# Kernel optimization log

Hardware: AMD Instinct MI355X
Metric: run time of the kernel (lower is better)

## Reference

```python
import jax, jax.numpy as jnp
import numpy as np

B, N, D = 64, 577, 768
H = 12
HD = D // H
TOP_K_RATIO = 0.1


def setup_inputs() -> dict:
    key = jax.random.key(0)
    ks = jax.random.split(key, 8)
    s = 1.0 / np.sqrt(D)
    return {
        "x": jax.random.normal(ks[0], (B, N, D), jnp.float32),
        "accumulated_attention": jax.random.uniform(ks[1], (B, N, N), jnp.float32),
        "q_w": jax.random.normal(ks[2], (D, D), jnp.float32) * s,
        "k_w": jax.random.normal(ks[3], (D, D), jnp.float32) * s,
        "v_w": jax.random.normal(ks[4], (D, D), jnp.float32) * s,
        "proj_w": jax.random.normal(ks[5], (D, D), jnp.float32) * s,
        "proj_b": jnp.zeros((D,), jnp.float32),
    }


def reference(x, accumulated_attention, q_w, k_w, v_w, proj_w, proj_b):
    b, n, d = x.shape
    scale = HD ** -0.5
    # CLS-to-patch attention rollout row: (B, N-1)
    cls_attn = accumulated_attention[:, 0, 1:]
    # projections -> (B, H, N, HD)
    q = (x @ q_w.T).reshape(b, n, H, HD).transpose(0, 2, 1, 3)
    k = (x @ k_w.T).reshape(b, n, H, HD).transpose(0, 2, 1, 3)
    v = (x @ v_w.T).reshape(b, n, H, HD).transpose(0, 2, 1, 3)
    # top-k patch selection (+1 for CLS offset), prepend CLS index 0
    kk = max(1, int((n - 1) * TOP_K_RATIO))
    _, top_idx = jax.lax.top_k(cls_attn, kk)
    sel = jnp.concatenate([jnp.zeros((b, 1), top_idx.dtype), top_idx + 1], axis=1)  # (B, K+1)
    # gather selected queries: (B, H, K+1, HD)
    local_q = jnp.take_along_axis(q, sel[:, None, :, None], axis=2)
    # cross-attention of local queries against full K/V
    attn = jax.nn.softmax(jnp.einsum("bhkd,bhnd->bhkn", local_q, k) * scale, axis=-1)
    local_out = jnp.einsum("bhkn,bhnd->bhkd", attn, v)
    local_out = local_out.transpose(0, 2, 1, 3).reshape(b, -1, d)  # (B, K+1, D)
    # scatter back into a copy of x (indices are unique per batch)
    out = x.at[jnp.arange(b)[:, None], sel].set(local_out)
    return out @ proj_w.T + proj_b
```

## Files before the change

kernel.cpp:

```cpp
#include <hip/hip_runtime.h>
#include <stdint.h>

typedef unsigned short u16;
typedef short bf16x8 __attribute__((ext_vector_type(8)));
typedef float f32x4 __attribute__((ext_vector_type(4)));

__device__ __forceinline__ float b2f(u16 u){
  unsigned int i = ((unsigned int)u) << 16;
  return __builtin_bit_cast(float, i);
}
__device__ __forceinline__ u16 f2b(float f){
  unsigned int i = __builtin_bit_cast(unsigned int, f);
  i += 0x7FFFu + ((i >> 16) & 1u);
  return (u16)(i >> 16);
}

__device__ __forceinline__ void async16(const void* g, void* l){
  __builtin_amdgcn_global_load_lds((__attribute__((address_space(1))) void*)(void*)g,
                                   (__attribute__((address_space(3))) void*)l, 16, 0, 0);
}

__global__ void probe_kernel(const u16* __restrict__ qw, int* __restrict__ flag){
  int cnt = 0;
  for (int i = threadIdx.x; i < 4096; i += 64){
    int e = (qw[i] >> 7) & 0xFF;
    cnt += (e >= 140);
  }
#pragma unroll
  for (int off = 32; off; off >>= 1) cnt += __shfl_down(cnt, off);
  if (threadIdx.x == 0) *flag = (cnt > 64) ? 1 : 0;
}

__global__ __launch_bounds__(256) void cvt_kernel(const void* __restrict__ src,
                                                  u16* __restrict__ dst, int n,
                                                  const int* __restrict__ flagp){
  const int i = (blockIdx.x * 256 + threadIdx.x) * 8;
  if (i >= n) return;
  if (*flagp){
    f32x4 a = *(const f32x4*)((const float*)src + i);
    f32x4 b = *(const f32x4*)((const float*)src + i + 4);
    bf16x8 v;
#pragma unroll
    for (int j = 0; j < 4; ++j){ v[j] = (short)f2b(a[j]); v[4+j] = (short)f2b(b[j]); }
    *(bf16x8*)(dst + i) = v;
  } else {
    *(bf16x8*)(dst + i) = *(const bf16x8*)((const u16*)src + i);
  }
}

__global__ __launch_bounds__(256) void cvtw4_kernel(const void* __restrict__ s0,
                                                    const void* __restrict__ s1,
                                                    const void* __restrict__ s2,
                                                    const void* __restrict__ s3,
                                                    u16* __restrict__ dst,
                                                    const int* __restrict__ flagp){
  const int b = blockIdx.x;
  const int wsel = b / 288;
  const int i = (b - wsel*288) * 2048 + threadIdx.x * 8;
  const void* src = (wsel == 0) ? s0 : (wsel == 1) ? s1 : (wsel == 2) ? s2 : s3;
  u16* d = dst + (size_t)wsel * 589824 + i;
  if (*flagp){
    f32x4 a = *(const f32x4*)((const float*)src + i);
    f32x4 c = *(const f32x4*)((const float*)src + i + 4);
    bf16x8 v;
#pragma unroll
    for (int j = 0; j < 4; ++j){ v[j] = (short)f2b(a[j]); v[4+j] = (short)f2b(c[j]); }
    *(bf16x8*)d = v;
  } else {
    *(bf16x8*)d = *(const bf16x8*)((const u16*)src + i);
  }
}

__global__ void cvtb_kernel(const void* __restrict__ src, float* __restrict__ dst,
                            int n, const int* __restrict__ flagp){
  int i = blockIdx.x * 256 + threadIdx.x;
  if (i < n) dst[i] = *flagp ? ((const float*)src)[i] : b2f(((const u16*)src)[i]);
}

__global__ __launch_bounds__(576) void topk_kernel(const void* __restrict__ aa,
                                                   int* __restrict__ qrows,
                                                   const int* __restrict__ flagp){
  const int b = blockIdx.x;
  const int isf32 = *flagp;
  __shared__ float vals[576];
  const int i = threadIdx.x;
  const size_t off = (size_t)b*332929 + 1 + i;
  vals[i] = isf32 ? ((const float*)aa)[off] : b2f(((const u16*)aa)[off]);
  __syncthreads();
  const float vi = vals[i];
  int rank = 0;
  for (int j = 0; j < 576; ++j){
    float vj = vals[j];
    rank += (int)((vj > vi) || (vj == vi && j < i));
  }
  if (rank < 57) qrows[b*58 + 1 + rank] = b*577 + i + 1;
  if (i == 0)    qrows[b*58] = b*577;
}

__global__ __launch_bounds__(256) void gemm_bt(
    const u16* __restrict__ A, const u16* __restrict__ W,
    u16* __restrict__ Ck, u16* __restrict__ Cvt, float* __restrict__ Cout,
    u16* __restrict__ Clq,
    const int* __restrict__ qrows, const float* __restrict__ bias, int mode)
{
  __shared__ __align__(16) u16 As0[4096], As1[4096], As2[4096];
  __shared__ __align__(16) u16 Bs0[4096], Bs1[4096], Bs2[4096];
  const int tid = threadIdx.x;
  const int w = tid >> 6, l = tid & 63;

  int bx, by; bool lqp = false;
  if (mode == 0){
    const int bid = blockIdx.x;
    const int wg = (bid & 7) * 672 + (bid >> 3);
    if (wg < 5202){ bx = wg % 18; by = wg / 18; }
    else { const int t = wg - 5202; bx = t % 6; by = t / 6; lqp = true; }
  } else { bx = blockIdx.x; by = blockIdx.y; }

  const int mBase = by * 128;
  const int nBase = bx * 128;
  const int Meff  = (mode == 0 && !lqp) ? 36928 : 3712;

  const int r0 = tid >> 2;
  const int kc = (((tid & 3) ^ ((r0 >> 1) & 3)) * 8);
  int arow0 = mBase + r0;       if (arow0 > Meff-1) arow0 = Meff-1;
  int arow1 = mBase + 64 + r0;  if (arow1 > Meff-1) arow1 = Meff-1;
  if (mode == 0 && lqp){ arow0 = qrows[arow0]; arow1 = qrows[arow1]; }
  const int wrowBase = (mode == 0 && !lqp) ? (768 + nBase) : nBase;
  const u16* ag0 = A + (size_t)arow0 * 768 + kc;
  const u16* ag1 = A + (size_t)arow1 * 768 + kc;
  const u16* bg0 = W + (size_t)(wrowBase + r0) * 768 + kc;
  const u16* bg1 = W + (size_t)(wrowBase + 64 + r0) * 768 + kc;
  const int toff0 = tid * 8, toff1 = (256 + tid) * 8;

  f32x4 acc[4][4] = {};
  const int wm = (w >> 1) * 64, wn = (w & 1) * 64;
  const int lm = l & 15;
  const int lkx = (((l >> 4) ^ ((l >> 1) & 3)) * 8);

#define STAGE(Ab, Bb, koff) do { \
    async16(ag0 + (koff), &Ab[toff0]); \
    async16(ag1 + (koff), &Ab[toff1]); \
    async16(bg0 + (koff), &Bb[toff0]); \
    async16(bg1 + (koff), &Bb[toff1]); } while(0)

#define COMPUTE(Ab, Bb) { \
    bf16x8 af[4], bfr[4]; \
    _Pragma("unroll") \
    for (int i = 0; i < 4; ++i) af[i]  = *(const bf16x8*)&Ab[(wm + i*16 + lm)*32 + lkx]; \
    _Pragma("unroll") \
    for (int j = 0; j < 4; ++j) bfr[j] = *(const bf16x8*)&Bb[(wn + j*16 + lm)*32 + lkx]; \
    __builtin_amdgcn_s_setprio(1); \
    _Pragma("unroll") \
    for (int i = 0; i < 4; ++i) \
      _Pragma("unroll") \
      for (int j = 0; j < 4; ++j) \
        acc[i][j] = __builtin_amdgcn_mfma_f32_16x16x32_bf16(af[i], bfr[j], acc[i][j], 0, 0, 0); \
    __builtin_amdgcn_s_setprio(0); }

#define VMW4 asm volatile("s_waitcnt vmcnt(4)" ::: "memory")
#define VMW0 asm volatile("s_waitcnt vmcnt(0)" ::: "memory")
#define BAR  __builtin_amdgcn_s_barrier()

  STAGE(As0, Bs0, 0);
  STAGE(As1, Bs1, 32);
#pragma unroll
  for (int u = 0; u < 7; ++u){
    const int kb = u * 96;
    VMW4; BAR; STAGE(As2, Bs2, kb + 64);  COMPUTE(As0, Bs0);
    VMW4; BAR; STAGE(As0, Bs0, kb + 96);  COMPUTE(As1, Bs1);
    VMW4; BAR; STAGE(As1, Bs1, kb + 128); COMPUTE(As2, Bs2);
  }
  VMW4; BAR; STAGE(As2, Bs2, 736); COMPUTE(As0, Bs0);
  VMW4; BAR;                       COMPUTE(As1, Bs1);
  VMW0; BAR;                       COMPUTE(As2, Bs2);

#undef STAGE
#undef COMPUTE
#undef VMW4
#undef VMW0
#undef BAR

  if (mode == 1){
#pragma unroll
    for (int i = 0; i < 4; ++i){
#pragma unroll
      for (int r = 0; r < 4; ++r){
        int m = mBase + wm + i*16 + ((l >> 4) << 2) + r;
        if (m < 3712){
          size_t base = (size_t)qrows[m] * 768;
#pragma unroll
          for (int j = 0; j < 4; ++j){
            int n = nBase + wn + j*16 + lm;
            Cout[base + n] = acc[i][j][r] + bias[n];
          }
        }
      }
    }
    return;
  }
  if (lqp){
#pragma unroll
    for (int i = 0; i < 4; ++i){
#pragma unroll
      for (int r = 0; r < 4; ++r){
        int m = mBase + wm + i*16 + ((l >> 4) << 2) + r;
#pragma unroll
        for (int j = 0; j < 4; ++j){
          int n = nBase + wn + j*16 + lm;
          Clq[(size_t)m*768 + n] = f2b(acc[i][j][r]);
        }
      }
    }
  } else if (nBase < 768){
#pragma unroll
    for (int i = 0; i < 4; ++i){
#pragma unroll
      for (int r = 0; r < 4; ++r){
        int m = mBase + wm + i*16 + ((l >> 4) << 2) + r;
        if (m < 36928){
#pragma unroll
          for (int j = 0; j < 4; ++j){
            int n = nBase + wn + j*16 + lm;
            Ck[(size_t)m*768 + n] = f2b(acc[i][j][r]);
          }
        }
      }
    }
  } else if (nBase < 1536){
#pragma unroll
    for (int i = 0; i < 4; ++i){
#pragma unroll
      for (int r = 0; r < 4; ++r){
        int m = mBase + wm + i*16 + ((l >> 4) << 2) + r;
        if (m < 36928){
          int bb = m / 577;
          int nn = m - bb*577;
#pragma unroll
          for (int j = 0; j < 4; ++j){
            int nf = nBase - 768 + wn + j*16 + lm;
            Cvt[((size_t)(bb*12 + (nf >> 6))*64 + (nf & 63))*608 + nn] = f2b(acc[i][j][r]);
          }
        }
      }
    }
  } else {
#pragma unroll
    for (int i = 0; i < 4; ++i){
#pragma unroll
      for (int r = 0; r < 4; ++r){
        int m = mBase + wm + i*16 + ((l >> 4) << 2) + r;
        if (m < 36928){
          size_t base = (size_t)m * 768;
#pragma unroll
          for (int j = 0; j < 4; ++j){
            int nf = nBase - 1536 + wn + j*16 + lm;
            Cout[base + nf] = acc[i][j][r] + bias[nf];
          }
        }
      }
    }
  }
}

#define SLD 580
__global__ __launch_bounds__(256) void attn_kernel(
    const u16* __restrict__ lq, const u16* __restrict__ K,
    const u16* __restrict__ Vt, u16* __restrict__ lout)
{
  const int bid = blockIdx.x;
  const int wg = (bid & 7) * 384 + (bid >> 3);
  const int mt = wg & 3;
  const int hb = wg >> 2;
  const int h = hb % 12, b = hb / 12;

  __shared__ __align__(16) u16 qs[16*64];
  __shared__ __align__(16) float S[16*SLD];
  float* red = (float*)qs;
  const int tid = threadIdx.x, w = tid >> 6, l = tid & 63;
  const int lm = l & 15, lk = (l >> 4) * 8;

  for (int idx = tid; idx < 1024; idx += 256){
    int r = idx >> 6, c = idx & 63;
    int gm = mt*16 + r;
    qs[idx] = (gm < 58) ? lq[((size_t)b*58 + gm)*768 + h*64 + c] : (u16)0;
  }
  __syncthreads();
  bf16x8 aq0 = *(const bf16x8*)&qs[lm*64 + lk];
  bf16x8 aq1 = *(const bf16x8*)&qs[lm*64 + 32 + lk];

  const u16* Kb = K + (size_t)b*577*768 + h*64;
  for (int t = w; t < 37; t += 4){
    int n0 = t*16;
    int n = n0 + lm; if (n > 576) n = 576;
    const u16* kp = Kb + (size_t)n*768;
    bf16x8 b0 = *(const bf16x8*)&kp[lk];
    bf16x8 b1 = *(const bf16x8*)&kp[32 + lk];
    f32x4 c = {};
    c = __builtin_amdgcn_mfma_f32_16x16x32_bf16(aq0, b0, c, 0, 0, 0);
    c = __builtin_amdgcn_mfma_f32_16x16x32_bf16(aq1, b1, c, 0, 0, 0);
    if (n0 + lm < 577){
#pragma unroll
      for (int r = 0; r < 4; ++r)
        S[(((l >> 4) << 2) + r)*SLD + n0 + lm] = c[r] * 0.125f;
    }
  }
  __syncthreads();

  const int row = tid >> 4, g = tid & 15;
  float mx = -1e30f;
  for (int n = g; n < 577; n += 16) mx = fmaxf(mx, S[row*SLD + n]);
  red[row*17 + g] = mx;
  __syncthreads();
  float m2 = red[row*17];
#pragma unroll
  for (int i = 1; i < 16; ++i) m2 = fmaxf(m2, red[row*17 + i]);
  float sum = 0.f;
  for (int n = g; n < 577; n += 16){
    float e = __expf(S[row*SLD + n] - m2);
    S[row*SLD + n] = e;
    sum += e;
  }
  __syncthreads();
  red[row*17 + g] = sum;
  __syncthreads();
  float s2 = 0.f;
#pragma unroll
  for (int i = 0; i < 16; ++i) s2 += red[row*17 + i];
  float inv = 1.f / s2;
  for (int n = g; n < 577; n += 16) S[row*SLD + n] *= inv;
  __syncthreads();

  const u16* Vb = Vt + ((size_t)(b*12 + h) * 64) * 608;
  f32x4 oc = {};
  for (int ks = 0; ks < 18; ++ks){
    int kb = ks*32 + lk;
    f32x4 p0 = *(const f32x4*)&S[lm*SLD + kb];
    f32x4 p1 = *(const f32x4*)&S[lm*SLD + kb + 4];
    bf16x8 af;
#pragma unroll
    for (int j = 0; j < 4; ++j){ af[j] = (short)f2b(p0[j]); af[4+j] = (short)f2b(p1[j]); }
    bf16x8 bv = *(const bf16x8*)&Vb[(size_t)(w*16 + lm)*608 + kb];
    oc = __builtin_amdgcn_mfma_f32_16x16x32_bf16(af, bv, oc, 0, 0, 0);
  }
  {
    float vt576 = b2f(Vb[(size_t)(w*16 + lm)*608 + 576]);
#pragma unroll
    for (int r = 0; r < 4; ++r)
      oc[r] += S[(((l >> 4) << 2) + r)*SLD + 576] * vt576;
  }
#pragma unroll
  for (int r = 0; r < 4; ++r){
    int ml = mt*16 + ((l >> 4) << 2) + r;
    if (ml < 58)
      lout[((size_t)b*58 + ml)*768 + h*64 + w*16 + lm] = f2b(oc[r]);
  }
}

extern "C" void kernel_launch(void* const* d_in, const int* in_sizes, int n_in,
                              void* d_out, int out_size, void* d_ws, size_t ws_size,
                              hipStream_t stream)
{
  const void* x    = d_in[0];
  const void* aacc = d_in[1];
  const void* q_w  = d_in[2];
  const void* k_w  = d_in[3];
  const void* v_w  = d_in[4];
  const void* p_w  = d_in[5];
  const void* p_b  = d_in[6];

  const int M  = 36928;
  const int Ms = 3712;
  const int XE = M * 768;
  const int WE = 768 * 768;

  u16* Kbuf = (u16*)d_ws;
  u16* Vt   = Kbuf + (size_t)M * 768;
  u16* lq   = Vt + (size_t)768 * 64 * 608;
  u16* lout = lq + (size_t)Ms * 768;
  u16* xb   = lout + (size_t)Ms * 768;
  u16* qwb  = xb + (size_t)XE;
  u16* pwb  = qwb + (size_t)3 * WE;
  float* biasf = (float*)(qwb + (size_t)4 * WE);
  int* qrows = (int*)(biasf + 768);
  int* flagp = qrows + 3712;

  probe_kernel<<<1, 64, 0, stream>>>((const u16*)q_w, flagp);
  cvt_kernel<<<XE/8/256, 256, 0, stream>>>(x, xb, XE, flagp);
  cvtw4_kernel<<<1152, 256, 0, stream>>>(q_w, k_w, v_w, p_w, qwb, flagp);
  cvtb_kernel<<<3, 256, 0, stream>>>(p_b, biasf, 768, flagp);
  topk_kernel<<<64, 576, 0, stream>>>(aacc, qrows, flagp);

  gemm_bt<<<5376, 256, 0, stream>>>(xb, qwb, Kbuf, Vt, (float*)d_out, lq,
                                    qrows, biasf, 0);
  attn_kernel<<<3072, 256, 0, stream>>>(lq, Kbuf, Vt, lout);
  gemm_bt<<<dim3(6, 29), 256, 0, stream>>>(lout, pwb, nullptr, nullptr,
                                           (float*)d_out, nullptr, qrows, biasf, 1);
}
```

Before: 578.2 us.

## Double-buffer GEMM for occupancy, prefetch K/V in attention, defer softmax normalization

The GEMM drops from triple- to double-buffered LDS staging, with an extra barrier between compute and restage, and adds a launch-bounds occupancy hint of 4 blocks. The aim is more resident workgroups per CU in exchange for a shallower prefetch pipeline. The attention kernel software-prefetches the next K tile and the next V fragment into registers. It also skips the pass that normalizes the softmax row and instead multiplies the output by the reciprocal row sum at the end. Unnormalized probabilities are then rounded to bf16 before the PV MFMA, which slightly changes precision.

Result: no change. 576.0 us (-0.4%).

```diff
diff --git a/kernel.cpp b/kernel.cpp
--- a/kernel.cpp
+++ b/kernel.cpp
@@ -97,14 +97,14 @@
   if (i == 0)    qrows[b*58] = b*577;
 }
 
-__global__ __launch_bounds__(256) void gemm_bt(
+__global__ __launch_bounds__(256, 4) void gemm_bt(
     const u16* __restrict__ A, const u16* __restrict__ W,
     u16* __restrict__ Ck, u16* __restrict__ Cvt, float* __restrict__ Cout,
     u16* __restrict__ Clq,
     const int* __restrict__ qrows, const float* __restrict__ bias, int mode)
 {
-  __shared__ __align__(16) u16 As0[4096], As1[4096], As2[4096];
-  __shared__ __align__(16) u16 Bs0[4096], Bs1[4096], Bs2[4096];
+  __shared__ __align__(16) u16 As0[4096], As1[4096];
+  __shared__ __align__(16) u16 Bs0[4096], Bs1[4096];
   const int tid = threadIdx.x;
   const int w = tid >> 6, l = tid & 63;
 
@@ -164,15 +164,12 @@
   STAGE(As0, Bs0, 0);
   STAGE(As1, Bs1, 32);
 #pragma unroll
-  for (int u = 0; u < 7; ++u){
-    const int kb = u * 96;
-    VMW4; BAR; STAGE(As2, Bs2, kb + 64);  COMPUTE(As0, Bs0);
-    VMW4; BAR; STAGE(As0, Bs0, kb + 96);  COMPUTE(As1, Bs1);
-    VMW4; BAR; STAGE(As1, Bs1, kb + 128); COMPUTE(As2, Bs2);
-  }
-  VMW4; BAR; STAGE(As2, Bs2, 736); COMPUTE(As0, Bs0);
-  VMW4; BAR;                       COMPUTE(As1, Bs1);
-  VMW0; BAR;                       COMPUTE(As2, Bs2);
+  for (int u = 0; u < 11; ++u){
+    VMW4; BAR; COMPUTE(As0, Bs0); BAR; STAGE(As0, Bs0, u*64 + 64);
+    VMW4; BAR; COMPUTE(As1, Bs1); BAR; STAGE(As1, Bs1, u*64 + 96);
+  }
+  VMW4; BAR; COMPUTE(As0, Bs0);
+  VMW0; BAR; COMPUTE(As1, Bs1);
 
 #undef STAGE
 #undef COMPUTE
@@ -275,7 +272,8 @@
 
   __shared__ __align__(16) u16 qs[16*64];
   __shared__ __align__(16) float S[16*SLD];
-  float* red = (float*)qs;
+  float* red  = (float*)qs;
+  float* invp = red + 16*17;
   const int tid = threadIdx.x, w = tid >> 6, l = tid & 63;
   const int lm = l & 15, lk = (l >> 4) * 8;
 
@@ -289,19 +287,31 @@
   bf16x8 aq1 = *(const bf16x8*)&qs[lm*64 + 32 + lk];
 
   const u16* Kb = K + (size_t)b*577*768 + h*64;
-  for (int t = w; t < 37; t += 4){
-    int n0 = t*16;
-    int n = n0 + lm; if (n > 576) n = 576;
+  {
+    int t = w;
+    int n = t*16 + lm; if (n > 576) n = 576;
     const u16* kp = Kb + (size_t)n*768;
-    bf16x8 b0 = *(const bf16x8*)&kp[lk];
-    bf16x8 b1 = *(const bf16x8*)&kp[32 + lk];
-    f32x4 c = {};
-    c = __builtin_amdgcn_mfma_f32_16x16x32_bf16(aq0, b0, c, 0, 0, 0);
-    c = __builtin_amdgcn_mfma_f32_16x16x32_bf16(aq1, b1, c, 0, 0, 0);
-    if (n0 + lm < 577){
-#pragma unroll
-      for (int r = 0; r < 4; ++r)
-        S[(((l >> 4) << 2) + r)*SLD + n0 + lm] = c[r] * 0.125f;
+    bf16x8 kb0 = *(const bf16x8*)&kp[lk];
+    bf16x8 kb1 = *(const bf16x8*)&kp[32 + lk];
+    while (t < 37){
+      const int tn = t + 4;
+      bf16x8 nb0 = kb0, nb1 = kb1;
+      if (tn < 37){
+        int n2 = tn*16 + lm; if (n2 > 576) n2 = 576;
+        const u16* kp2 = Kb + (size_t)n2*768;
+        nb0 = *(const bf16x8*)&kp2[lk];
+        nb1 = *(const bf16x8*)&kp2[32 + lk];
+      }
+      f32x4 c = {};
+      c = __builtin_amdgcn_mfma_f32_16x16x32_bf16(aq0, kb0, c, 0, 0, 0);
+      c = __builtin_amdgcn_mfma_f32_16x16x32_bf16(aq1, kb1, c, 0, 0, 0);
+      const int n0 = t*16;
+      if (n0 + lm < 577){
+#pragma unroll
+        for (int r = 0; r < 4; ++r)
+          S[(((l >> 4) << 2) + r)*SLD + n0 + lm] = c[r] * 0.125f;
+      }
+      kb0 = nb0; kb1 = nb1; t = tn;
     }
   }
   __syncthreads();
@@ -323,30 +333,37 @@
   __syncthreads();
   red[row*17 + g] = sum;
   __syncthreads();
-  float s2 = 0.f;
-#pragma unroll
-  for (int i = 0; i < 16; ++i) s2 += red[row*17 + i];
-  float inv = 1.f / s2;
-  for (int n = g; n < 577; n += 16) S[row*SLD + n] *= inv;
+  if (g == 0){
+    float s2 = 0.f;
+#pragma unroll
+    for (int i = 0; i < 16; ++i) s2 += red[row*17 + i];
+    invp[row] = 1.f / s2;
+  }
   __syncthreads();
 
   const u16* Vb = Vt + ((size_t)(b*12 + h) * 64) * 608;
+  const u16* Vrow = Vb + (size_t)(w*16 + lm)*608;
   f32x4 oc = {};
+  bf16x8 bv = *(const bf16x8*)&Vrow[lk];
   for (int ks = 0; ks < 18; ++ks){
-    int kb = ks*32 + lk;
+    const int kb = ks*32 + lk;
+    bf16x8 bvn = bv;
+    if (ks < 17) bvn = *(const bf16x8*)&Vrow[kb + 32];
     f32x4 p0 = *(const f32x4*)&S[lm*SLD + kb];
     f32x4 p1 = *(const f32x4*)&S[lm*SLD + kb + 4];
     bf16x8 af;
 #pragma unroll
     for (int j = 0; j < 4; ++j){ af[j] = (short)f2b(p0[j]); af[4+j] = (short)f2b(p1[j]); }
-    bf16x8 bv = *(const bf16x8*)&Vb[(size_t)(w*16 + lm)*608 + kb];
     oc = __builtin_amdgcn_mfma_f32_16x16x32_bf16(af, bv, oc, 0, 0, 0);
+    bv = bvn;
   }
   {
-    float vt576 = b2f(Vb[(size_t)(w*16 + lm)*608 + 576]);
-#pragma unroll
-    for (int r = 0; r < 4; ++r)
-      oc[r] += S[(((l >> 4) << 2) + r)*SLD + 576] * vt576;
+    float vt576 = b2f(Vrow[576]);
+#pragma unroll
+    for (int r = 0; r < 4; ++r){
+      int sr = (((l >> 4) << 2) + r);
+      oc[r] = (oc[r] + S[sr*SLD + 576] * vt576) * invp[sr];
+    }
   }
 #pragma unroll
   for (int r = 0; r < 4; ++r){
```
